# Optimization experiments

Measured on AMD Instinct MI355X. Metric: run time of the kernel, lower is better.

The kernel has to match this reference:

```python
import jax, jax.numpy as jnp
import numpy as np

B, T, D_IN, D_OUT, N_FILT, MAX_T = 4, 2048, 512, 512, 24, 2048


def _hankel_filters(max_t: int, k: int) -> np.ndarray:
    # Z_{ij} = 2 / ((i+j)^3 - (i+j)), 1-indexed; top-|eig| eigenvectors
    idx = np.arange(1, max_t + 1, dtype=np.float64)
    ij = idx[None, :] + idx[:, None]
    Z = 2.0 / (ij ** 3 - ij)
    w, v = np.linalg.eigh(Z)
    top = np.argsort(-np.abs(w))[:k]
    return v[:, top].astype(np.float32)  # (max_t, k)


def setup_inputs() -> dict:
    key = jax.random.key(0)
    kx, km = jax.random.split(key)
    x = jax.random.normal(kx, (B, T, D_IN), dtype=jnp.float32)
    filters = jnp.asarray(_hankel_filters(MAX_T, N_FILT))  # (MAX_T, N)
    # nn.Linear weight is (d_out, d_in); stacked -> (N, d_out, d_in)
    scale = 1.0 / np.sqrt(D_IN)
    M_weights = jax.random.uniform(km, (N_FILT, D_OUT, D_IN), dtype=jnp.float32,
                                   minval=-scale, maxval=scale)
    return {"x": x, "filters": filters, "M_weights": M_weights}


def reference(x, filters, M_weights):
    Tlen = x.shape[1]
    phi = filters[:Tlen]                       # (T, N)
    phi_e = phi[None, :, :, None]              # (1, T, N, 1)
    weighted = phi_e * x[:, :, None, :]        # (B, T, N, D_in)
    csum = jnp.cumsum(weighted, axis=1)        # causal cumulative projection
    # per-filter rectangular projection: (B,T,N,f) x (N,o,f) -> (B,T,N,o)
    modulated = jnp.einsum('btnf,nof->btno', csum, M_weights)
    return (phi_e * modulated).sum(axis=2)     # (B, T, D_out)
```

## Files before the change

kernel.cpp:

```cpp
#include <hip/hip_runtime.h>
#include <stdint.h>

#define BQ 4
#define TT 2048
#define DF 512
#define DOUT 512
#define NF 24
#define CHF 8

typedef __attribute__((ext_vector_type(8))) short short8;
typedef __attribute__((ext_vector_type(4))) float f32x4;

typedef __attribute__((address_space(3))) uint8_t       lds_u8;
typedef __attribute__((address_space(1))) const uint8_t glb_u8;

__device__ __forceinline__ float bf2f(unsigned short u) {
    union { unsigned int i; float f; } v; v.i = ((unsigned int)u) << 16; return v.f;
}
__device__ __forceinline__ unsigned short f2bf(float f) {
    union { float f; unsigned int i; } v; v.f = f;
    unsigned int r = v.i + 0x7FFFu + ((v.i >> 16) & 1u);
    return (unsigned short)(r >> 16);
}
__device__ __forceinline__ float lo16f(unsigned int u) { return __uint_as_float(u << 16); }
__device__ __forceinline__ float hi16f(unsigned int u) { return __uint_as_float(u & 0xffff0000u); }

__device__ __forceinline__ int plaus16(unsigned int h) {
    unsigned int e = (h >> 7) & 0xffu;
    return (e >= 97u && e <= 141u) || ((h & 0x7fffu) == 0u);
}

__global__ void k_detect(const unsigned int* __restrict__ X, int* __restrict__ flag)
{
    const int lane = threadIdx.x;
    int cnt = 0;
#pragma unroll
    for (int i = 0; i < 4; ++i) {
        unsigned int w = X[lane * 4 + i];
        cnt += (plaus16(w >> 16) && plaus16(w & 0xffffu)) ? 1 : 0;
    }
    for (int off = 32; off > 0; off >>= 1) cnt += __shfl_down(cnt, off);
    if (lane == 0) *flag = (cnt < 180) ? 1 : 0;
}

__global__ __launch_bounds__(256) void k_convf(
    const void* __restrict__ src, float* __restrict__ dst,
    const int* __restrict__ flag, int n)
{
    const int isf32 = *flag;
    int i = blockIdx.x * 256 + threadIdx.x;
    const int stride = gridDim.x * 256;
    for (; i < n; i += stride)
        dst[i] = isf32 ? ((const float*)src)[i]
                       : bf2f(((const unsigned short*)src)[i]);
}

__global__ __launch_bounds__(256) void k_prep(
    const void* __restrict__ X, const void* __restrict__ Mw,
    const void* __restrict__ Fil,
    unsigned short* __restrict__ Xbf, unsigned short* __restrict__ Mbf,
    float* __restrict__ Fw, int n4x, int n4m, int n4f)
{
    __shared__ int sflag;
    const int tid = threadIdx.x;
    if (tid < 64) {
        int cnt = 0;
        const unsigned int* Xu = (const unsigned int*)X;
#pragma unroll
        for (int i = 0; i < 4; ++i) {
            unsigned int wd = Xu[tid * 4 + i];
            cnt += (plaus16(wd >> 16) && plaus16(wd & 0xffffu)) ? 1 : 0;
        }
        for (int off = 32; off > 0; off >>= 1) cnt += __shfl_down(cnt, off);
        if (tid == 0) sflag = (cnt < 180) ? 1 : 0;
    }
    __syncthreads();
    const int isf32 = sflag;

    const int total = n4x + n4m + n4f;
    for (int i = blockIdx.x * 256 + tid; i < total; i += gridDim.x * 256) {
        if (i < n4x) {
            ushort4 o;
            if (isf32) {
                float4 v = ((const float4*)X)[i];
                o.x = f2bf(v.x); o.y = f2bf(v.y); o.z = f2bf(v.z); o.w = f2bf(v.w);
            } else {
                o = ((const ushort4*)X)[i];
            }
            ((ushort4*)Xbf)[i] = o;
        } else if (i < n4x + n4m) {
            const int j = i - n4x;
            ushort4 o;
            if (isf32) {
                float4 v = ((const float4*)Mw)[j];
                o.x = f2bf(v.x); o.y = f2bf(v.y); o.z = f2bf(v.z); o.w = f2bf(v.w);
            } else {
                o = ((const ushort4*)Mw)[j];
            }
            ((ushort4*)Mbf)[j] = o;
        } else {
            const int j = i - n4x - n4m;
            if (isf32) {
                ((float4*)Fw)[j] = ((const float4*)Fil)[j];
            } else {
                ushort4 u = ((const ushort4*)Fil)[j];
                ((float4*)Fw)[j] = make_float4(bf2f(u.x), bf2f(u.y),
                                               bf2f(u.z), bf2f(u.w));
            }
        }
    }
}

__global__ __launch_bounds__(256, 3) void k_gemm_fast(
    const unsigned short* __restrict__ X,
    const unsigned short* __restrict__ Mw,
    const float* __restrict__ Fw,
    unsigned short* __restrict__ Z,
    float* __restrict__ Cs,
    int r0)
{
    __shared__ unsigned short sAB[128 * 136];
    __shared__ float sPhi[128];
    unsigned short* const sC = sAB;

    const int tid  = threadIdx.x;
    const int lane = tid & 63;
    const int w    = tid >> 6;
    const int wm   = w & 1, wn = w >> 1;

    const int gx = gridDim.x, gy = gridDim.y;
    const int nwg = gx * gy * gridDim.z;
    int lid = blockIdx.x + gx * (blockIdx.y + gy * blockIdx.z);
    int swz = lid;
    if ((nwg & 7) == 0) swz = (lid & 7) * (nwg >> 3) + (lid >> 3);
    const int tm   = swz % gx;
    const int rest = swz / gx;
    const int on0  = (rest % gy) * 128;
    const int n    = rest / gy;

    const int rowg0 = r0 + tm * 128;
    if (tid < 128)
        sPhi[tid] = Fw[((rowg0 + tid) & (TT - 1)) * NF + n];

    const unsigned short* Ag = X + (size_t)rowg0 * DF;
    const unsigned short* Bg = Mw + (size_t)n * DOUT * DF + (size_t)on0 * DF;

    auto stage = [&](int kt, int buf) {
        const unsigned short* Ak = Ag + kt * 32;
        const unsigned short* Bk = Bg + kt * 32;
        lds_u8* base = (lds_u8*)sAB + buf * 16384;
#pragma unroll
        for (int i = 0; i < 2; ++i) {
            const int cbase = i * 256 + w * 64;
            const int c = cbase + lane;
            const int r = c >> 2, qs = c & 3;
            const int qg = qs ^ ((r >> 1) & 3);
            __builtin_amdgcn_global_load_lds(
                (const glb_u8*)(Ak + (size_t)r * DF + qg * 8),
                base + cbase * 16, 16, 0, 0);
            __builtin_amdgcn_global_load_lds(
                (const glb_u8*)(Bk + (size_t)r * DF + qg * 8),
                base + 8192 + cbase * 16, 16, 0, 0);
        }
    };

    f32x4 acc[4][4];
#pragma unroll
    for (int i = 0; i < 4; i++)
#pragma unroll
        for (int j = 0; j < 4; j++) acc[i][j] = (f32x4){0.f, 0.f, 0.f, 0.f};

    stage(0, 0);
    __syncthreads();

    const int lr = lane & 15;
    const int q  = lane >> 4;
    const int qsw = (q ^ ((lr >> 1) & 3)) * 8;

    for (int kt = 0; kt < DF / 32; ++kt) {
        const int cur = kt & 1;
        if (kt < DF / 32 - 1) stage(kt + 1, cur ^ 1);

        const unsigned short* sAc = sAB + cur * 8192;
        const unsigned short* sBc = sAc + 4096;
        short8 a[4], b[4];
#pragma unroll
        for (int i = 0; i < 4; i++)
            a[i] = *(const short8*)&sAc[(wm * 64 + i * 16 + lr) * 32 + qsw];
#pragma unroll
        for (int j = 0; j < 4; j++)
            b[j] = *(const short8*)&sBc[(wn * 64 + j * 16 + lr) * 32 + qsw];
#pragma unroll
        for (int i = 0; i < 4; i++)
#pragma unroll
            for (int j = 0; j < 4; j++)
                acc[i][j] = __builtin_amdgcn_mfma_f32_16x16x32_bf16(
                    a[i], b[j], acc[i][j], 0, 0, 0);

        __syncthreads();
    }

    const int rb = (lane >> 4) * 4;
#pragma unroll
    for (int i = 0; i < 4; i++)
#pragma unroll
        for (int j = 0; j < 4; j++)
#pragma unroll
            for (int r = 0; r < 4; r++) {
                int row = wm * 64 + i * 16 + rb + r;
                sC[row * 136 + wn * 64 + j * 16 + (lane & 15)] =
                    f2bf(acc[i][j][r] * sPhi[row]);
            }
    __syncthreads();

#pragma unroll
    for (int it = 0; it < 8; ++it) {
        int row = it * 16 + (tid >> 4);
        int col = (tid & 15) * 8;
        uint4 v = *(const uint4*)&sC[row * 136 + col];
        *(uint4*)&Z[((size_t)(tm * 128 + row) * NF + n) * 512 + on0 + col] = v;
    }

    {
        const int ci  = tid >> 4;
        const int col = (tid & 15) * 8;
        float s0=0.f,s1=0.f,s2=0.f,s3=0.f,s4=0.f,s5=0.f,s6=0.f,s7=0.f;
#pragma unroll
        for (int r = 0; r < CHF; ++r) {
            uint4 v = *(const uint4*)&sC[(ci * CHF + r) * 136 + col];
            s0 += lo16f(v.x); s1 += hi16f(v.x);
            s2 += lo16f(v.y); s3 += hi16f(v.y);
            s4 += lo16f(v.z); s5 += hi16f(v.z);
            s6 += lo16f(v.w); s7 += hi16f(v.w);
        }
        float* cp = &Cs[((size_t)(tm * 16 + ci) * NF + n) * 512 + on0 + col];
        *(float4*)cp       = make_float4(s0, s1, s2, s3);
        *(float4*)(cp + 4) = make_float4(s4, s5, s6, s7);
    }
}

__global__ __launch_bounds__(256, 2) void k_gemm(
    const void* __restrict__ Xv, const void* __restrict__ Mv,
    const void* __restrict__ Fv, const int* __restrict__ flag,
    unsigned short* __restrict__ Z, int r0, int o0, int W)
{
    __shared__ unsigned short sA[128 * 32];
    __shared__ unsigned short sB[128 * 32];
    __shared__ unsigned short sC[128 * 136];
    __shared__ float sPhi[128];

    const int isf32 = *flag;
    const int tid  = threadIdx.x;
    const int lane = tid & 63;
    const int w    = tid >> 6;
    const int wm   = w & 1, wn = w >> 1;
    const int tm   = blockIdx.x;
    const int on0  = o0 + blockIdx.y * 128;
    const int n    = blockIdx.z;

    const int rowg0 = r0 + tm * 128;
    if (tid < 128) {
        int t = (rowg0 + tid) & (TT - 1);
        sPhi[tid] = isf32 ? ((const float*)Fv)[t * NF + n]
                          : bf2f(((const unsigned short*)Fv)[t * NF + n]);
    }

    const unsigned short* Ah = (const unsigned short*)Xv + (size_t)rowg0 * DF;
    const unsigned short* Bh = (const unsigned short*)Mv +
        (size_t)n * DOUT * DF + (size_t)on0 * DF;
    const float* Af = (const float*)Xv + (size_t)rowg0 * DF;
    const float* Bf = (const float*)Mv + (size_t)n * DOUT * DF + (size_t)on0 * DF;

    f32x4 acc[4][4];
#pragma unroll
    for (int i = 0; i < 4; i++)
#pragma unroll
        for (int j = 0; j < 4; j++) acc[i][j] = (f32x4){0.f, 0.f, 0.f, 0.f};

    for (int kt = 0; kt < DF / 32; ++kt) {
        __syncthreads();
        if (!isf32) {
            const unsigned short* Ak = Ah + kt * 32;
            const unsigned short* Bk = Bh + kt * 32;
#pragma unroll
            for (int i = 0; i < 2; ++i) {
                const int c = i * 256 + tid;
                const int r = c >> 2, cc = (c & 3) * 8;
                *(short8*)&sA[r * 32 + cc] = *(const short8*)(Ak + (size_t)r * DF + cc);
                *(short8*)&sB[r * 32 + cc] = *(const short8*)(Bk + (size_t)r * DF + cc);
            }
        } else {
            const float* Ak = Af + kt * 32;
            const float* Bk = Bf + kt * 32;
#pragma unroll
            for (int i = 0; i < 2; ++i) {
                const int c = i * 256 + tid;
                const int r = c >> 2, cc = (c & 3) * 8;
                float4 a0 = *(const float4*)(Ak + (size_t)r * DF + cc);
                float4 a1 = *(const float4*)(Ak + (size_t)r * DF + cc + 4);
                float4 b0 = *(const float4*)(Bk + (size_t)r * DF + cc);
                float4 b1 = *(const float4*)(Bk + (size_t)r * DF + cc + 4);
                short8 sa, sb;
                sa[0]=(short)f2bf(a0.x); sa[1]=(short)f2bf(a0.y);
                sa[2]=(short)f2bf(a0.z); sa[3]=(short)f2bf(a0.w);
                sa[4]=(short)f2bf(a1.x); sa[5]=(short)f2bf(a1.y);
                sa[6]=(short)f2bf(a1.z); sa[7]=(short)f2bf(a1.w);
                sb[0]=(short)f2bf(b0.x); sb[1]=(short)f2bf(b0.y);
                sb[2]=(short)f2bf(b0.z); sb[3]=(short)f2bf(b0.w);
                sb[4]=(short)f2bf(b1.x); sb[5]=(short)f2bf(b1.y);
                sb[6]=(short)f2bf(b1.z); sb[7]=(short)f2bf(b1.w);
                *(short8*)&sA[r * 32 + cc] = sa;
                *(short8*)&sB[r * 32 + cc] = sb;
            }
        }
        __syncthreads();

        const int lr = lane & 15;
        const int lk = (lane >> 4) * 8;
        short8 a[4], b[4];
#pragma unroll
        for (int i = 0; i < 4; i++)
            a[i] = *(const short8*)&sA[(wm * 64 + i * 16 + lr) * 32 + lk];
#pragma unroll
        for (int j = 0; j < 4; j++)
            b[j] = *(const short8*)&sB[(wn * 64 + j * 16 + lr) * 32 + lk];
#pragma unroll
        for (int i = 0; i < 4; i++)
#pragma unroll
            for (int j = 0; j < 4; j++)
                acc[i][j] = __builtin_amdgcn_mfma_f32_16x16x32_bf16(
                    a[i], b[j], acc[i][j], 0, 0, 0);
    }

    const int rb = (lane >> 4) * 4;
#pragma unroll
    for (int i = 0; i < 4; i++)
#pragma unroll
        for (int j = 0; j < 4; j++)
#pragma unroll
            for (int r = 0; r < 4; r++) {
                int row = wm * 64 + i * 16 + rb + r;
                sC[row * 136 + wn * 64 + j * 16 + (lane & 15)] =
                    f2bf(acc[i][j][r] * sPhi[row]);
            }
    __syncthreads();
#pragma unroll
    for (int it = 0; it < 8; ++it) {
        int row = it * 16 + (tid >> 4);
        int col = (tid & 15) * 8;
        uint4 v = *(const uint4*)&sC[row * 136 + col];
        *(uint4*)&Z[((size_t)(tm * 128 + row) * NF + n) * W + (on0 - o0) + col] = v;
    }
}

__global__ __launch_bounds__(256, 2) void k_csum(
    const unsigned short* __restrict__ Z, float* __restrict__ Cs,
    int W, int CHs)
{
    const int c = blockIdx.x, n = blockIdx.y, tid = threadIdx.x;
    const unsigned short* p = Z + ((size_t)(c * CHs) * NF + n) * W + tid * 2;
    float sx = 0.f, sy = 0.f;
#pragma unroll 8
    for (int t = 0; t < CHs; ++t) {
        unsigned int u = *(const unsigned int*)(p + (size_t)t * NF * W);
        sx += lo16f(u);
        sy += hi16f(u);
    }
    float2* q = (float2*)&Cs[((size_t)c * NF + n) * W + tid * 2];
    *q = make_float2(sx, sy);
}

__global__ __launch_bounds__(256, 4) void k_prefix(
    float* __restrict__ Cs, float* __restrict__ Gc,
    int W, int rr, int nch, int nbat)
{
    const int tid  = threadIdx.x;
    const int lane = tid & 63;
    const int obw  = W >> 7;
    const int tasks = nbat * NF * obw;
    const int gw = blockIdx.x * 4 + (tid >> 6);
    if (gw >= tasks) return;
    const int perB = NF * obw;
    const int b    = gw / perB;
    const int rest = gw % perB;
    const int n    = rest / obw;
    const int ob   = rest % obw;
    const int opair = ob * 64 + lane;

    float* base = Cs + (size_t)b * nch * NF * W + (size_t)n * W + opair * 2;
    const size_t cstride = (size_t)NF * W;

    float cx = 0.f, cy = 0.f;
    if (nbat == 1 && rr != 0) {
        float2 g = *(const float2*)&Gc[(size_t)n * DOUT + opair * 2];
        cx = g.x; cy = g.y;
    }

    int c = 0;
    if (nch >= 16) {
        float2 v[8], w2[8];
#pragma unroll
        for (int k = 0; k < 8; ++k) v[k] = *(float2*)(base + (size_t)k * cstride);
        for (; c + 16 <= nch; c += 8) {
#pragma unroll
            for (int k = 0; k < 8; ++k)
                w2[k] = *(float2*)(base + (size_t)(c + 8 + k) * cstride);
#pragma unroll
            for (int k = 0; k < 8; ++k) {
                float2* p = (float2*)(base + (size_t)(c + k) * cstride);
                float2 t = v[k];
                *p = make_float2(cx, cy);
                cx += t.x; cy += t.y;
                v[k] = w2[k];
            }
        }
#pragma unroll
        for (int k = 0; k < 8; ++k) {
            float2* p = (float2*)(base + (size_t)(c + k) * cstride);
            float2 t = v[k];
            *p = make_float2(cx, cy);
            cx += t.x; cy += t.y;
        }
        c += 8;
    }
    for (; c < nch; ++c) {
        float2* p = (float2*)(base + (size_t)c * cstride);
        float2 t = *p;
        *p = make_float2(cx, cy);
        cx += t.x; cy += t.y;
    }

    if (nbat == 1)
        *(float2*)&Gc[(size_t)n * DOUT + opair * 2] = make_float2(cx, cy);
}

#define JLIST(F) F(0) F(1) F(2) F(3) F(4) F(5)

__global__ __launch_bounds__(256, 4) void k_scan(
    const unsigned short* __restrict__ Z, const float* __restrict__ Cs,
    const float* __restrict__ Fw, float* __restrict__ Out,
    int r0, int o0, int W, int CHs)
{
    __shared__ float sPhi[32 * NF];
    __shared__ float4 sP[4][8][64];
    const int cg = blockIdx.x, tid = threadIdx.x;
    const int g = tid >> 6, op = tid & 63;
    const int ng0 = g * 6;
    const int c4  = (blockIdx.y * 64 + op) * 4;
    const int act = (c4 + 4 <= W);
    const int c4u = act ? c4 : (W - 4);
    const int t0g = r0 + cg * CHs;
    const int t0 = t0g & (TT - 1);
    for (int i = tid; i < CHs * NF; i += 256)
        sPhi[i] = Fw[(t0 + i / NF) * NF + (i % NF)];
    __syncthreads();

#define DECLG(j) float gA##j, gB##j, gC##j, gD##j;
    JLIST(DECLG)
#define INITG(j) { float4 v = *(const float4*)&Cs[((size_t)cg * NF + ng0 + j) * W + c4u]; \
                   gA##j = v.x; gB##j = v.y; gC##j = v.z; gD##j = v.w; }
    JLIST(INITG)

    const unsigned short* zp = Z + ((size_t)cg * CHs * NF + ng0) * W + c4u;
    float* outb = Out + (size_t)t0g * DOUT + o0 + c4;
    for (int tb = 0; tb < CHs; tb += 8) {
#pragma unroll
        for (int tt = 0; tt < 8; ++tt) {
            float a0 = 0.f, a1 = 0.f, a2 = 0.f, a3 = 0.f;
            const float* php = &sPhi[(tb + tt) * NF + ng0];
#define UPDG(j) { uint2 u = *(const uint2*)(zp + (size_t)j * W); \
                  gA##j += lo16f(u.x); gB##j += hi16f(u.x); \
                  gC##j += lo16f(u.y); gD##j += hi16f(u.y); \
                  float ph = php[j]; \
                  a0 += ph * gA##j; a1 += ph * gB##j; \
                  a2 += ph * gC##j; a3 += ph * gD##j; }
            JLIST(UPDG)
            sP[g][tt][op] = make_float4(a0, a1, a2, a3);
            zp += (size_t)NF * W;
        }
        __syncthreads();
#pragma unroll
        for (int k = 0; k < 2; ++k) {
            const int tt = g * 2 + k;
            float4 p0 = sP[0][tt][op], p1 = sP[1][tt][op],
                   p2 = sP[2][tt][op], p3 = sP[3][tt][op];
            if (act)
                *(float4*)(outb + (size_t)(tb + tt) * DOUT) =
                    make_float4(p0.x + p1.x + p2.x + p3.x,
                                p0.y + p1.y + p2.y + p3.y,
                                p0.z + p1.z + p2.z + p3.z,
                                p0.w + p1.w + p2.w + p3.w);
        }
        __syncthreads();
    }
}

extern "C" void kernel_launch(void* const* d_in, const int* in_sizes, int n_in,
                              void* d_out, int out_size, void* d_ws, size_t ws_size,
                              hipStream_t stream)
{
    const void* X = d_in[0]; const void* Fil = d_in[1]; const void* Mw = d_in[2];
    for (int i = 0; i < n_in && i < 3; ++i) {
        if (in_sizes[i] == BQ * TT * DF)        X   = d_in[i];
        else if (in_sizes[i] == TT * NF)        Fil = d_in[i];
        else if (in_sizes[i] == NF * DOUT * DF) Mw  = d_in[i];
    }
    float* Out = (float*)d_out;

    const size_t offF = 256;
    const size_t nbF  = (size_t)TT * NF * 4;
    const size_t off0 = offF + nbF;
    const size_t nbX  = (size_t)BQ * TT * DF * 2;
    const size_t nbM  = (size_t)NF * DOUT * DF * 2;
    const size_t nbGc = (size_t)NF * DOUT * 4;

    int* flag = (int*)d_ws;
    float* Fw = (float*)((char*)d_ws + offF);

    const int n4x = BQ * TT * DF / 4;
    const int n4m = NF * DOUT * DF / 4;
    const int n4f = TT * NF / 4;

    for (int G = BQ; G >= 2; G >>= 1) {
        const size_t zB  = (size_t)G * TT * NF * 512 * 2;
        const size_t csB = (size_t)(G * TT / CHF) * NF * 512 * 4;
        if (off0 + nbX + nbM + zB + csB > ws_size) continue;

        unsigned short* Xbf = (unsigned short*)((char*)d_ws + off0);
        unsigned short* Mbf = (unsigned short*)((char*)Xbf + nbX);
        unsigned short* Z   = (unsigned short*)((char*)Mbf + nbM);
        float* Cs = (float*)((char*)Z + zB);

        hipLaunchKernelGGL(k_prep, dim3(2048), dim3(256), 0, stream,
                           X, Mw, Fil, Xbf, Mbf, Fw, n4x, n4m, n4f);

        const int nch = TT / CHF;
        for (int b0 = 0; b0 < BQ; b0 += G) {
            hipLaunchKernelGGL(k_gemm_fast, dim3(G * TT / 128, 4, NF), dim3(256),
                               0, stream, Xbf, Mbf, Fw, Z, Cs, b0 * TT);
            hipLaunchKernelGGL(k_prefix, dim3((G * NF * 4 + 3) / 4), dim3(256),
                               0, stream, Cs, (float*)nullptr, 512, 0, nch, G);
            hipLaunchKernelGGL(k_scan, dim3(G * nch, 2), dim3(256), 0, stream,
                               Z, Cs, Fw, Out, b0 * TT, 0, 512, CHF);
        }
        return;
    }

    {
        static const int rts[5] = {2048, 1024, 512, 256, 128};
        int RT = 0;
        for (int ri = 0; ri < 5; ++ri) {
            size_t need = off0 + nbX + nbM
                        + (size_t)rts[ri] * NF * 512 * 2
                        + (size_t)(rts[ri] / CHF) * NF * 512 * 4 + nbGc;
            if (need <= ws_size) { RT = rts[ri]; break; }
        }
        if (RT > 0) {
            unsigned short* Xbf = (unsigned short*)((char*)d_ws + off0);
            unsigned short* Mbf = (unsigned short*)((char*)Xbf + nbX);
            unsigned short* Z   = (unsigned short*)((char*)Mbf + nbM);
            float* Cs = (float*)((char*)Z + (size_t)RT * NF * 512 * 2);
            float* Gc = (float*)((char*)Cs + (size_t)(RT / CHF) * NF * 512 * 4);

            hipLaunchKernelGGL(k_prep, dim3(2048), dim3(256), 0, stream,
                               X, Mw, Fil, Xbf, Mbf, Fw, n4x, n4m, n4f);

            const int nrr = TT / RT, nch = RT / CHF;
            for (int b = 0; b < BQ; ++b) {
                for (int rr = 0; rr < nrr; ++rr) {
                    const int r0 = b * TT + rr * RT;
                    hipLaunchKernelGGL(k_gemm_fast, dim3(RT / 128, 4, NF), dim3(256),
                                       0, stream, Xbf, Mbf, Fw, Z, Cs, r0);
                    hipLaunchKernelGGL(k_prefix, dim3((NF * 4 + 3) / 4), dim3(256),
                                       0, stream, Cs, Gc, 512, rr, nch, 1);
                    hipLaunchKernelGGL(k_scan, dim3(nch, 2), dim3(256), 0, stream,
                                       Z, Cs, Fw, Out, r0, 0, 512, CHF);
                }
            }
            return;
        }
    }

    hipLaunchKernelGGL(k_detect, dim3(1), dim3(64), 0, stream,
                       (const unsigned int*)X, flag);
    hipLaunchKernelGGL(k_convf, dim3(192), dim3(256), 0, stream,
                       Fil, Fw, flag, TT * NF);

    static const int cRT[7] = {2048, 1024, 512, 256, 128, 128, 128};
    static const int cW[7]  = {512, 512, 512, 512, 512, 256, 128};
    int RTs = 128, W = 128;
    for (int ci = 0; ci < 7; ++ci) {
        size_t need = off0 + (size_t)cRT[ci] * NF * cW[ci] * 2
                    + (size_t)(cRT[ci] / 32) * NF * cW[ci] * 4 + nbGc;
        if (need <= ws_size) { RTs = cRT[ci]; W = cW[ci]; break; }
    }
    unsigned short* Z = (unsigned short*)((char*)d_ws + off0);
    float* Cs = (float*)((char*)Z + (size_t)RTs * NF * W * 2);
    float* Gc = (float*)((char*)Cs + (size_t)(RTs / 32) * NF * W * 4);

    const int nrr = TT / RTs, nch = RTs / 32;
    for (int b = 0; b < BQ; ++b) {
        for (int o0 = 0; o0 < DOUT; o0 += W) {
            for (int rr = 0; rr < nrr; ++rr) {
                const int r0 = b * TT + rr * RTs;
                hipLaunchKernelGGL(k_gemm, dim3(RTs / 128, W / 128, NF), dim3(256),
                                   0, stream, X, Mw, Fil, flag, Z, r0, o0, W);
                hipLaunchKernelGGL(k_csum, dim3(nch, NF), dim3(W / 2), 0, stream,
                                   Z, Cs, W, 32);
                hipLaunchKernelGGL(k_prefix, dim3((NF * (W / 128) + 3) / 4), dim3(256),
                                   0, stream, Cs, Gc, W, rr, nch, 1);
                hipLaunchKernelGGL(k_scan, dim3(nch, (W + 255) / 256), dim3(256),
                                   0, stream, Z, Cs, Fw, Out, r0, o0, W, 32);
            }
        }
    }
}
```

Baseline: 333.5 us.

## Parallelize prefix over chunks per block, halve scan columns, drop GEMM swizzle

The prefix kernel now gives each (batch, filter, column-block) task a whole block. Its four waves each reduce a quarter of the chunks, combine the partial sums through LDS, then each scans its quarter, instead of one wave walking all chunks serially. The scan kernel now handles two output columns per thread instead of four, with twice the column blocks and a higher occupancy hint, to expose more parallelism and lower register pressure. The GEMM drops its XCD-style block swizzle in favour of direct blockIdx mapping, which may hurt L2 locality across chiplets.

```diff
diff --git a/kernel.cpp b/kernel.cpp
--- a/kernel.cpp
+++ b/kernel.cpp
@@ -127,16 +127,9 @@
     const int lane = tid & 63;
     const int w    = tid >> 6;
     const int wm   = w & 1, wn = w >> 1;
-
-    const int gx = gridDim.x, gy = gridDim.y;
-    const int nwg = gx * gy * gridDim.z;
-    int lid = blockIdx.x + gx * (blockIdx.y + gy * blockIdx.z);
-    int swz = lid;
-    if ((nwg & 7) == 0) swz = (lid & 7) * (nwg >> 3) + (lid >> 3);
-    const int tm   = swz % gx;
-    const int rest = swz / gx;
-    const int on0  = (rest % gy) * 128;
-    const int n    = rest / gy;
+    const int tm   = blockIdx.x;
+    const int on0  = blockIdx.y * 128;
+    const int n    = blockIdx.z;
 
     const int rowg0 = r0 + tm * 128;
     if (tid < 128)
@@ -374,13 +367,12 @@
     float* __restrict__ Cs, float* __restrict__ Gc,
     int W, int rr, int nch, int nbat)
 {
+    __shared__ float2 sPart[4][64];
     const int tid  = threadIdx.x;
-    const int lane = tid & 63;
+    const int wv   = tid >> 6, lane = tid & 63;
     const int obw  = W >> 7;
-    const int tasks = nbat * NF * obw;
-    const int gw = blockIdx.x * 4 + (tid >> 6);
-    if (gw >= tasks) return;
     const int perB = NF * obw;
+    const int gw   = blockIdx.x;
     const int b    = gw / perB;
     const int rest = gw % perB;
     const int n    = rest / obw;
@@ -389,29 +381,45 @@
 
     float* base = Cs + (size_t)b * nch * NF * W + (size_t)n * W + opair * 2;
     const size_t cstride = (size_t)NF * W;
+    const int Q  = nch >> 2;
+    const int c0 = wv * Q;
+    const int end = c0 + Q;
+
+    float sx = 0.f, sy = 0.f;
+    for (int c = c0; c < end; ++c) {
+        float2 v = *(const float2*)(base + (size_t)c * cstride);
+        sx += v.x; sy += v.y;
+    }
+    sPart[wv][lane] = make_float2(sx, sy);
+    __syncthreads();
 
     float cx = 0.f, cy = 0.f;
     if (nbat == 1 && rr != 0) {
-        float2 g = *(const float2*)&Gc[(size_t)n * DOUT + opair * 2];
-        cx = g.x; cy = g.y;
-    }
-
-    int c = 0;
-    if (nch >= 16) {
-        float2 v[8], w2[8];
-#pragma unroll
-        for (int k = 0; k < 8; ++k) v[k] = *(float2*)(base + (size_t)k * cstride);
-        for (; c + 16 <= nch; c += 8) {
+        float2 gv = *(const float2*)&Gc[(size_t)n * DOUT + opair * 2];
+        cx = gv.x; cy = gv.y;
+    }
+    for (int w2 = 0; w2 < wv; ++w2) {
+        float2 p = sPart[w2][lane];
+        cx += p.x; cy += p.y;
+    }
+
+    int c = c0;
+    if (Q >= 16) {
+        float2 v[8], nx[8];
+#pragma unroll
+        for (int k = 0; k < 8; ++k)
+            v[k] = *(float2*)(base + (size_t)(c + k) * cstride);
+        for (; c + 16 <= end; c += 8) {
 #pragma unroll
             for (int k = 0; k < 8; ++k)
-                w2[k] = *(float2*)(base + (size_t)(c + 8 + k) * cstride);
+                nx[k] = *(float2*)(base + (size_t)(c + 8 + k) * cstride);
 #pragma unroll
             for (int k = 0; k < 8; ++k) {
                 float2* p = (float2*)(base + (size_t)(c + k) * cstride);
                 float2 t = v[k];
                 *p = make_float2(cx, cy);
                 cx += t.x; cy += t.y;
-                v[k] = w2[k];
+                v[k] = nx[k];
             }
         }
 #pragma unroll
@@ -423,73 +431,68 @@
         }
         c += 8;
     }
-    for (; c < nch; ++c) {
+    for (; c < end; ++c) {
         float2* p = (float2*)(base + (size_t)c * cstride);
         float2 t = *p;
         *p = make_float2(cx, cy);
         cx += t.x; cy += t.y;
     }
 
-    if (nbat == 1)
+    if (nbat == 1 && wv == 3)
         *(float2*)&Gc[(size_t)n * DOUT + opair * 2] = make_float2(cx, cy);
 }
 
 #define JLIST(F) F(0) F(1) F(2) F(3) F(4) F(5)
 
-__global__ __launch_bounds__(256, 4) void k_scan(
+__global__ __launch_bounds__(256, 8) void k_scan(
     const unsigned short* __restrict__ Z, const float* __restrict__ Cs,
     const float* __restrict__ Fw, float* __restrict__ Out,
     int r0, int o0, int W, int CHs)
 {
     __shared__ float sPhi[32 * NF];
-    __shared__ float4 sP[4][8][64];
+    __shared__ float2 sP[4][8][64];
     const int cg = blockIdx.x, tid = threadIdx.x;
     const int g = tid >> 6, op = tid & 63;
     const int ng0 = g * 6;
-    const int c4  = (blockIdx.y * 64 + op) * 4;
-    const int act = (c4 + 4 <= W);
-    const int c4u = act ? c4 : (W - 4);
+    const int c2  = (blockIdx.y * 64 + op) * 2;
+    const int act = (c2 + 2 <= W);
+    const int c2u = act ? c2 : (W - 2);
     const int t0g = r0 + cg * CHs;
     const int t0 = t0g & (TT - 1);
     for (int i = tid; i < CHs * NF; i += 256)
         sPhi[i] = Fw[(t0 + i / NF) * NF + (i % NF)];
     __syncthreads();
 
-#define DECLG(j) float gA##j, gB##j, gC##j, gD##j;
+#define DECLG(j) float gx##j, gy##j;
     JLIST(DECLG)
-#define INITG(j) { float4 v = *(const float4*)&Cs[((size_t)cg * NF + ng0 + j) * W + c4u]; \
-                   gA##j = v.x; gB##j = v.y; gC##j = v.z; gD##j = v.w; }
+#define INITG(j) { float2 v = *(const float2*)&Cs[((size_t)cg * NF + ng0 + j) * W + c2u]; \
+                   gx##j = v.x; gy##j = v.y; }
     JLIST(INITG)
 
-    const unsigned short* zp = Z + ((size_t)cg * CHs * NF + ng0) * W + c4u;
-    float* outb = Out + (size_t)t0g * DOUT + o0 + c4;
+    const unsigned short* zp = Z + ((size_t)cg * CHs * NF + ng0) * W + c2u;
+    float* outb = Out + (size_t)t0g * DOUT + o0 + c2;
     for (int tb = 0; tb < CHs; tb += 8) {
 #pragma unroll
         for (int tt = 0; tt < 8; ++tt) {
-            float a0 = 0.f, a1 = 0.f, a2 = 0.f, a3 = 0.f;
+            float ax = 0.f, ay = 0.f;
             const float* php = &sPhi[(tb + tt) * NF + ng0];
-#define UPDG(j) { uint2 u = *(const uint2*)(zp + (size_t)j * W); \
-                  gA##j += lo16f(u.x); gB##j += hi16f(u.x); \
-                  gC##j += lo16f(u.y); gD##j += hi16f(u.y); \
-                  float ph = php[j]; \
-                  a0 += ph * gA##j; a1 += ph * gB##j; \
-                  a2 += ph * gC##j; a3 += ph * gD##j; }
+#define UPDG(j) { unsigned int u = *(const unsigned int*)(zp + (size_t)j * W); \
+                  gx##j += lo16f(u); gy##j += hi16f(u); \
+                  float ph = php[j]; ax += ph * gx##j; ay += ph * gy##j; }
             JLIST(UPDG)
-            sP[g][tt][op] = make_float4(a0, a1, a2, a3);
+            sP[g][tt][op] = make_float2(ax, ay);
             zp += (size_t)NF * W;
         }
         __syncthreads();
 #pragma unroll
         for (int k = 0; k < 2; ++k) {
             const int tt = g * 2 + k;
-            float4 p0 = sP[0][tt][op], p1 = sP[1][tt][op],
+            float2 p0 = sP[0][tt][op], p1 = sP[1][tt][op],
                    p2 = sP[2][tt][op], p3 = sP[3][tt][op];
             if (act)
-                *(float4*)(outb + (size_t)(tb + tt) * DOUT) =
-                    make_float4(p0.x + p1.x + p2.x + p3.x,
-                                p0.y + p1.y + p2.y + p3.y,
-                                p0.z + p1.z + p2.z + p3.z,
-                                p0.w + p1.w + p2.w + p3.w);
+                *(float2*)(outb + (size_t)(tb + tt) * DOUT) =
+                    make_float2(p0.x + p1.x + p2.x + p3.x,
+                                p0.y + p1.y + p2.y + p3.y);
         }
         __syncthreads();
     }
@@ -538,9 +541,9 @@
         for (int b0 = 0; b0 < BQ; b0 += G) {
             hipLaunchKernelGGL(k_gemm_fast, dim3(G * TT / 128, 4, NF), dim3(256),
                                0, stream, Xbf, Mbf, Fw, Z, Cs, b0 * TT);
-            hipLaunchKernelGGL(k_prefix, dim3((G * NF * 4 + 3) / 4), dim3(256),
+            hipLaunchKernelGGL(k_prefix, dim3(G * NF * 4), dim3(256),
                                0, stream, Cs, (float*)nullptr, 512, 0, nch, G);
-            hipLaunchKernelGGL(k_scan, dim3(G * nch, 2), dim3(256), 0, stream,
+            hipLaunchKernelGGL(k_scan, dim3(G * nch, 4), dim3(256), 0, stream,
                                Z, Cs, Fw, Out, b0 * TT, 0, 512, CHF);
         }
         return;
@@ -571,9 +574,9 @@
                     const int r0 = b * TT + rr * RT;
                     hipLaunchKernelGGL(k_gemm_fast, dim3(RT / 128, 4, NF), dim3(256),
                                        0, stream, Xbf, Mbf, Fw, Z, Cs, r0);
-                    hipLaunchKernelGGL(k_prefix, dim3((NF * 4 + 3) / 4), dim3(256),
+                    hipLaunchKernelGGL(k_prefix, dim3(NF * 4), dim3(256),
                                        0, stream, Cs, Gc, 512, rr, nch, 1);
-                    hipLaunchKernelGGL(k_scan, dim3(nch, 2), dim3(256), 0, stream,
+                    hipLaunchKernelGGL(k_scan, dim3(nch, 4), dim3(256), 0, stream,
                                        Z, Cs, Fw, Out, r0, 0, 512, CHF);
                 }
             }
@@ -607,9 +610,9 @@
                                    0, stream, X, Mw, Fil, flag, Z, r0, o0, W);
                 hipLaunchKernelGGL(k_csum, dim3(nch, NF), dim3(W / 2), 0, stream,
                                    Z, Cs, W, 32);
-                hipLaunchKernelGGL(k_prefix, dim3((NF * (W / 128) + 3) / 4), dim3(256),
+                hipLaunchKernelGGL(k_prefix, dim3(NF * (W / 128)), dim3(256),
                                    0, stream, Cs, Gc, W, rr, nch, 1);
-                hipLaunchKernelGGL(k_scan, dim3(nch, (W + 255) / 256), dim3(256),
+                hipLaunchKernelGGL(k_scan, dim3(nch, W / 128), dim3(256),
                                    0, stream, Z, Cs, Fw, Out, r0, o0, W, 32);
             }
         }
```

New measurement: 319.4 us. 4.2% less time.
